# Kernel optimization log

Measured on AMD Instinct MI355X. Metric: run time of the kernel, lower is better.

Reference implementation:

```python
import jax, jax.numpy as jnp
import numpy as np

N = 65536
E = 524288
G = 8192
HID = 512


def setup_inputs() -> dict:
    key = jax.random.key(0)
    ks = jax.random.split(key, 10)
    v_x_raw = jax.random.normal(ks[0], (N, 3), dtype=jnp.float32)
    H_decoded = jax.random.normal(ks[1], (N, HID), dtype=jnp.float32)
    x_t = 2.0 * jax.random.normal(ks[2], (N, 3), dtype=jnp.float32)
    row = jax.random.randint(ks[3], (E,), 0, N)
    # avoid self edges (fully_connect_edges excludes i==j)
    col = (row + 1 + jax.random.randint(ks[4], (E,), 0, N - 1)) % N
    edges = jnp.stack([row, col]).astype(jnp.int64)
    gen_idx = (jnp.arange(G, dtype=jnp.int32) * (N // G)).astype(jnp.int32)
    gen_mask = jnp.zeros((N,), dtype=bool).at[gen_idx].set(True)
    W_proj = jax.random.normal(ks[5], (HID, HID // 2), dtype=jnp.float32) / np.sqrt(HID)
    b_proj = jnp.zeros((HID // 2,), dtype=jnp.float32)
    w_bond = jax.random.normal(ks[6], (HID // 2, 1), dtype=jnp.float32) / np.sqrt(HID // 2)
    b_bond = jnp.zeros((1,), dtype=jnp.float32)
    w_val = jax.random.normal(ks[7], (HID // 2, 1), dtype=jnp.float32) / np.sqrt(HID // 2)
    b_val = jnp.zeros((1,), dtype=jnp.float32)
    return {"v_x_raw": v_x_raw, "H_decoded": H_decoded, "x_t": x_t, "edges": edges,
            "gen_mask": gen_mask, "gen_idx": gen_idx, "W_proj": W_proj, "b_proj": b_proj,
            "w_bond": w_bond, "b_bond": b_bond, "w_val": w_val, "b_val": b_val}


def _constrained_velocity(v_x_raw, H_decoded, x_t, edges, gen_mask, gen_idx,
                          W_proj, b_proj, w_bond, b_bond, w_val, b_val):
    TARGET_LEN = 1.5   # target bond length
    MIN_DIST = 1.0     # clash cutoff
    EPS = 1e-8

    feat = H_decoded @ W_proj + b_proj                      # [N, HID//2]

    # --- bond length corrections: vectorized scatter-add over edges ---
    row, col = edges[0], edges[1]
    diff = x_t[row] - x_t[col]                              # [E, 3]
    dist = jnp.sqrt(jnp.maximum(jnp.sum(diff * diff, -1), 1e-24)) + EPS  # [E]
    edge_gate = (gen_mask[row] | gen_mask[col]).astype(x_t.dtype)
    # force_magnitude * force_direction = (d - L)/d * diff/d
    force = ((dist - TARGET_LEN) / (dist * dist) * edge_gate)[:, None] * diff  # [E,3]
    bond_corr = jnp.zeros_like(x_t).at[row].add(force).at[col].add(-force)

    # --- clash corrections: dense pairwise over generated atoms ---
    xg = x_t[gen_idx]                                       # [G, 3]
    sq = jnp.sum(xg * xg, -1)                               # [G]
    d2 = sq[:, None] + sq[None, :] - 2.0 * (xg @ xg.T)      # [G, G]
    d = jnp.sqrt(jnp.maximum(d2, 1e-24)) + EPS
    pair_mask = (d < MIN_DIST) & ~jnp.eye(xg.shape[0], dtype=bool)
    # (min - d)/d * (x_i - x_j)/d  ->  coef_ij * (x_i - x_j)
    coef = jnp.where(pair_mask, (MIN_DIST - d) / (d * d), 0.0)  # [G, G]
    corr_g = xg * jnp.sum(coef, 1, keepdims=True) - coef @ xg   # [G, 3]
    clash_corr = jnp.zeros_like(x_t).at[gen_idx].add(corr_g)

    bond_w = jax.nn.sigmoid(feat @ w_bond + b_bond)         # [N, 1]
    clash_w = jax.nn.sigmoid(feat @ w_val + b_val)          # [N, 1]
    return v_x_raw - 0.1 * bond_w * bond_corr - 0.05 * clash_w * clash_corr


def reference(v_x_raw, H_decoded, x_t, edges, gen_mask, gen_idx,
              W_proj, b_proj, w_bond, b_bond, w_val, b_val):
    return _constrained_velocity(v_x_raw, H_decoded, x_t, edges, gen_mask, gen_idx,
                                 W_proj, b_proj, w_bond, b_bond, w_val, b_val)
```

## Files before the change

kernel.cpp:

```cpp
#include <hip/hip_runtime.h>
#include <math.h>

#define HID_DIM  512
#define HIDH_DIM 256
#define ZBLOCKS  125
#define UBLOCKS  128
#define JC       256

__device__ __forceinline__ float dot4(float4 a, float4 b) {
    return a.x * b.x + a.y * b.y + a.z * b.z + a.w * b.w;
}

__global__ __launch_bounds__(256) void prep_kernel(
        const unsigned int* __restrict__ ew,
        const float* __restrict__ Wp,  const float* __restrict__ bp,
        const float* __restrict__ wb,  const float* __restrict__ bb,
        const float* __restrict__ wv,  const float* __restrict__ bv,
        const int* __restrict__ gen_idx, const float* __restrict__ x_t,
        float4* __restrict__ zbase, int zcount,
        float* __restrict__ u_bond, float* __restrict__ u_val,
        float* __restrict__ cvals, int* __restrict__ flag,
        float* __restrict__ xgx, float* __restrict__ xgy, float* __restrict__ xgz,
        unsigned char* __restrict__ mask, int* __restrict__ gpos,
        int n, int G, int GB) {
    int b = blockIdx.x, t = threadIdx.x;
    if (b < ZBLOCKS) {
        const float4 z = make_float4(0.f, 0.f, 0.f, 0.f);
        for (int i = b * 256 + t; i < zcount; i += ZBLOCKS * 256) zbase[i] = z;
    } else if (b == ZBLOCKS) {
        if (t < 64) {
            unsigned int v = ew[2 * t + 1];
            unsigned long long bl = __ballot(v == 0u);
            if (t == 0) flag[0] = (bl == 0xFFFFFFFFFFFFFFFFULL) ? 1 : 0;
        }
        __shared__ float s1[256], s2[256];
        float p1 = (t < HIDH_DIM) ? bp[t] * wb[t] : 0.f;
        float p2 = (t < HIDH_DIM) ? bp[t] * wv[t] : 0.f;
        s1[t] = p1; s2[t] = p2;
        __syncthreads();
        for (int s = 128; s > 0; s >>= 1) {
            if (t < s) { s1[t] += s1[t + s]; s2[t] += s2[t + s]; }
            __syncthreads();
        }
        if (t == 0) { cvals[0] = s1[0] + bb[0]; cvals[1] = s2[0] + bv[0]; }
    } else if (b < ZBLOCKS + 1 + UBLOCKS) {
        int w = t >> 6, lane = t & 63;
        int k = (b - ZBLOCKS - 1) * 4 + w;
        if (k < HID_DIM) {
            const float* wrow = Wp + (size_t)k * HIDH_DIM;
            float4 wr = *reinterpret_cast<const float4*>(wrow + lane * 4);
            float4 vb = *reinterpret_cast<const float4*>(wb + lane * 4);
            float4 vv = *reinterpret_cast<const float4*>(wv + lane * 4);
            float ub = dot4(wr, vb);
            float uv = dot4(wr, vv);
            #pragma unroll
            for (int off = 32; off > 0; off >>= 1) {
                ub += __shfl_down(ub, off, 64);
                uv += __shfl_down(uv, off, 64);
            }
            if (lane == 0) { u_bond[k] = ub; u_val[k] = uv; }
        }
    } else if (b < ZBLOCKS + 1 + UBLOCKS + GB) {
        int g = (b - ZBLOCKS - 1 - UBLOCKS) * 256 + t;
        if (g < G) {
            int idx = gen_idx[g];
            xgx[g] = x_t[3 * idx + 0];
            xgy[g] = x_t[3 * idx + 1];
            xgz[g] = x_t[3 * idx + 2];
        }
    } else {
        int base = ((b - ZBLOCKS - 1 - UBLOCKS - GB) * 256 + t) * 8;
        for (int k = 0; k < 8; ++k) {
            int i = base + k;
            if (i >= n) break;
            int lo = 0, hi = G - 1, g = -1;
            while (lo <= hi) {
                int mid = (lo + hi) >> 1;
                int v = gen_idx[mid];
                if (v == i) { g = mid; break; }
                if (v < i) lo = mid + 1; else hi = mid - 1;
            }
            mask[i] = (g >= 0) ? 1 : 0;
            if (g >= 0) gpos[i] = g;
        }
    }
}

__global__ __launch_bounds__(256) void mega_kernel(
        const float* __restrict__ H,
        const float* __restrict__ u_bond, const float* __restrict__ u_val,
        const float* __restrict__ cvals,
        const unsigned int* __restrict__ ew, const int* __restrict__ flag_p,
        const float* __restrict__ x_t, const unsigned char* __restrict__ mask,
        const float* __restrict__ xgx, const float* __restrict__ xgy,
        const float* __restrict__ xgz,
        float* __restrict__ bond_corr,
        float4* __restrict__ partials,
        float* __restrict__ bond_w, float* __restrict__ clash_w,
        int n, int E, int G, int NBG, int NBB, int NBC, int CXB) {
    __shared__ __align__(16) float sx[JC];
    __shared__ __align__(16) float sy[JC];
    __shared__ __align__(16) float sz[JC];
    int b = blockIdx.x, t = threadIdx.x;
    int stripe = b / 5, role = b - stripe * 5;

    if (role < 2) {
        int bb = stripe * 2 + role;
        if (bb >= NBG) return;
        int w = t >> 6, lane = t & 63;
        int row0 = bb * 32 + w * 8;
        int o0 = lane * 4, o1 = 256 + lane * 4;
        float4 ub0 = *reinterpret_cast<const float4*>(u_bond + o0);
        float4 ub1 = *reinterpret_cast<const float4*>(u_bond + o1);
        float4 uv0 = *reinterpret_cast<const float4*>(u_val + o0);
        float4 uv1 = *reinterpret_cast<const float4*>(u_val + o1);
        float c0 = cvals[0], c1 = cvals[1];
        #pragma unroll
        for (int r = 0; r < 8; r += 2) {
            int ra = row0 + r, rb = ra + 1;
            bool va = (ra < n), vb = (rb < n);
            const float* ha = H + (size_t)(va ? ra : 0) * HID_DIM;
            const float* hb = H + (size_t)(vb ? rb : 0) * HID_DIM;
            float4 a0 = *reinterpret_cast<const float4*>(ha + o0);
            float4 a1 = *reinterpret_cast<const float4*>(ha + o1);
            float4 b0 = *reinterpret_cast<const float4*>(hb + o0);
            float4 b1 = *reinterpret_cast<const float4*>(hb + o1);
            float sba = dot4(a0, ub0) + dot4(a1, ub1);
            float sva = dot4(a0, uv0) + dot4(a1, uv1);
            float sbb = dot4(b0, ub0) + dot4(b1, ub1);
            float svb = dot4(b0, uv0) + dot4(b1, uv1);
            #pragma unroll
            for (int off = 32; off > 0; off >>= 1) {
                sba += __shfl_down(sba, off, 64);
                sva += __shfl_down(sva, off, 64);
                sbb += __shfl_down(sbb, off, 64);
                svb += __shfl_down(svb, off, 64);
            }
            if (lane == 0) {
                if (va) {
                    bond_w[ra]  = 1.f / (1.f + expf(-(sba + c0)));
                    clash_w[ra] = 1.f / (1.f + expf(-(sva + c1)));
                }
                if (vb) {
                    bond_w[rb]  = 1.f / (1.f + expf(-(sbb + c0)));
                    clash_w[rb] = 1.f / (1.f + expf(-(svb + c1)));
                }
            }
        }
    } else if (role < 4) {
        int e = (stripe * 2 + role - 2) * 256 + t;
        if (e >= E) return;
        int f = flag_p[0];
        int row, col;
        if (f) {
            row = (int)ew[2 * (size_t)e];
            col = (int)ew[2 * ((size_t)E + e)];
        } else {
            row = (int)ew[e];
            col = (int)ew[(size_t)E + e];
        }
        if ((unsigned)row >= (unsigned)n || (unsigned)col >= (unsigned)n) return;
        if (!(mask[row] | mask[col])) return;
        float dx = x_t[3 * row + 0] - x_t[3 * col + 0];
        float dy = x_t[3 * row + 1] - x_t[3 * col + 1];
        float dz = x_t[3 * row + 2] - x_t[3 * col + 2];
        float d2 = dx * dx + dy * dy + dz * dz;
        float dist = sqrtf(fmaxf(d2, 1e-24f)) + 1e-8f;
        float s = (dist - 1.5f) / (dist * dist);
        float fx = s * dx, fy = s * dy, fz = s * dz;
        atomicAdd(&bond_corr[3 * row + 0],  fx);
        atomicAdd(&bond_corr[3 * row + 1],  fy);
        atomicAdd(&bond_corr[3 * row + 2],  fz);
        atomicAdd(&bond_corr[3 * col + 0], -fx);
        atomicAdd(&bond_corr[3 * col + 1], -fy);
        atomicAdd(&bond_corr[3 * col + 2], -fz);
    } else {
        int b2 = stripe;
        if (b2 >= NBC) return;
        int yc = b2 / CXB;
        int i  = (b2 - yc * CXB) * 256 + t;
        int j  = yc * JC + t;
        sx[t] = (j < G) ? xgx[j] : 1e30f;
        sy[t] = (j < G) ? xgy[j] : 1e30f;
        sz[t] = (j < G) ? xgz[j] : 1e30f;
        __syncthreads();
        if (i >= G) return;
        float xi = xgx[i], yi = xgy[i], zi = xgz[i];
        float csum = 0.f, cx = 0.f, cy = 0.f, cz = 0.f;
#define PROC(XS, YS, ZS) do {                                           \
            float dx = xi - (XS), dy = yi - (YS), dz = zi - (ZS);       \
            float d2 = fmaf(dx, dx, fmaf(dy, dy, dz * dz));             \
            float rm = __builtin_amdgcn_rsqf(d2);                       \
            float coef = fmaxf(fmaf(rm, rm, -rm), 0.0f);                \
            csum += coef;                                               \
            cx = fmaf(coef, (XS), cx);                                  \
            cy = fmaf(coef, (YS), cy);                                  \
            cz = fmaf(coef, (ZS), cz);                                  \
        } while (0)
        #pragma unroll 4
        for (int tt = 0; tt < JC; tt += 4) {
            float4 ax = *reinterpret_cast<const float4*>(&sx[tt]);
            float4 ay = *reinterpret_cast<const float4*>(&sy[tt]);
            float4 az = *reinterpret_cast<const float4*>(&sz[tt]);
            PROC(ax.x, ay.x, az.x);
            PROC(ax.y, ay.y, az.y);
            PROC(ax.z, ay.z, az.z);
            PROC(ax.w, ay.w, az.w);
        }
#undef PROC
        partials[(size_t)yc * G + i] = make_float4(csum, cx, cy, cz);
    }
}

__global__ void final_kernel(const float* __restrict__ v_x,
                             const float* __restrict__ bond_w,
                             const float* __restrict__ clash_w,
                             const float* __restrict__ bond_corr,
                             const unsigned char* __restrict__ mask,
                             const int* __restrict__ gpos,
                             const float* __restrict__ xgx,
                             const float* __restrict__ xgy,
                             const float* __restrict__ xgz,
                             const float4* __restrict__ partials,
                             float* __restrict__ out, int n, int G, int NYC) {
    int i = blockIdx.x * blockDim.x + threadIdx.x;
    if (i >= n) return;
    float bw = 0.1f * bond_w[i];
    float ox = v_x[3 * i + 0] - bw * bond_corr[3 * i + 0];
    float oy = v_x[3 * i + 1] - bw * bond_corr[3 * i + 1];
    float oz = v_x[3 * i + 2] - bw * bond_corr[3 * i + 2];
    if (mask[i]) {
        int g = gpos[i];
        float s = 0.f, vx = 0.f, vy = 0.f, vz = 0.f;
        for (int yc = 0; yc < NYC; ++yc) {
            float4 p = partials[(size_t)yc * G + g];
            s += p.x; vx += p.y; vy += p.z; vz += p.w;
        }
        float cw = 0.05f * clash_w[i];
        ox -= cw * (xgx[g] * s - vx);
        oy -= cw * (xgy[g] * s - vy);
        oz -= cw * (xgz[g] * s - vz);
    }
    out[3 * i + 0] = ox;
    out[3 * i + 1] = oy;
    out[3 * i + 2] = oz;
}

extern "C" void kernel_launch(void* const* d_in, const int* in_sizes, int n_in,
                              void* d_out, int out_size, void* d_ws, size_t ws_size,
                              hipStream_t stream) {
    const float* v_x_raw = (const float*)d_in[0];
    const float* H       = (const float*)d_in[1];
    const float* x_t     = (const float*)d_in[2];
    const unsigned int* edges_w = (const unsigned int*)d_in[3];
    const int* gen_idx   = (const int*)d_in[5];
    const float* W_proj  = (const float*)d_in[6];
    const float* b_proj  = (const float*)d_in[7];
    const float* w_bond  = (const float*)d_in[8];
    const float* b_bond  = (const float*)d_in[9];
    const float* w_val   = (const float*)d_in[10];
    const float* b_val   = (const float*)d_in[11];

    const int n = in_sizes[0] / 3;
    const int E = in_sizes[3] / 2;
    const int G = in_sizes[5];
    const int GB  = (G + 255) / 256;
    const int NYC = (G + JC - 1) / JC;

    char* ws = (char*)d_ws;
    float* bond_corr = (float*)(ws);
    size_t zbytes = (size_t)n * 12;
    size_t off = (zbytes + 15) & ~(size_t)15;
    int zcount = (int)(off / 16);
    unsigned char* mask = (unsigned char*)(ws + off); off += ((size_t)n + 15) & ~(size_t)15;
    int*   gpos    = (int*)(ws + off);                off += (size_t)n * 4;
    float* bond_w  = (float*)(ws + off);              off += (size_t)n * 4;
    float* clash_w = (float*)(ws + off);              off += (size_t)n * 4;
    float* u_bond  = (float*)(ws + off);              off += HID_DIM * 4;
    float* u_val   = (float*)(ws + off);              off += HID_DIM * 4;
    float* cvals   = (float*)(ws + off);              off += 16;
    int*   flag    = (int*)(ws + off);                off += 16;
    float* xgx     = (float*)(ws + off);              off += (size_t)G * 4;
    float* xgy     = (float*)(ws + off);              off += (size_t)G * 4;
    float* xgz     = (float*)(ws + off);              off += (size_t)G * 4;
    float4* partials = (float4*)(ws + off);           off += (size_t)NYC * G * 16;

    const int MB  = (n + 2047) / 2048;
    const int CXB = GB;
    const int NBC = CXB * NYC;
    const int NBG = (n + 31) / 32;
    const int NBB = (E + 255) / 256;

    int S = (NBG + 1) / 2;
    if ((NBB + 1) / 2 > S) S = (NBB + 1) / 2;
    if (NBC > S) S = NBC;

    prep_kernel<<<ZBLOCKS + 1 + UBLOCKS + GB + MB, 256, 0, stream>>>(
        edges_w, W_proj, b_proj, w_bond, b_bond, w_val, b_val,
        gen_idx, x_t, (float4*)ws, zcount,
        u_bond, u_val, cvals, flag, xgx, xgy, xgz, mask, gpos, n, G, GB);

    mega_kernel<<<S * 5, 256, 0, stream>>>(
        H, u_bond, u_val, cvals, edges_w, flag, x_t, mask,
        xgx, xgy, xgz, bond_corr, partials, bond_w, clash_w,
        n, E, G, NBG, NBB, NBC, CXB);

    final_kernel<<<(n + 255) / 256, 256, 0, stream>>>(
        v_x_raw, bond_w, clash_w, bond_corr, mask, gpos,
        xgx, xgy, xgz, partials, (float*)d_out, n, G, NYC);
}
```

Measured before the change: 98.86 us.

## Split gate GEMV out of mega kernel and rebalance bond/clash block interleave

Moves the H·u gate dot-products out of the interleaved mega kernel into a separate gate_kernel that uses half-wave (32-lane) reductions, with one row per half-wave and 8 rows per block. The remaining bond-scatter and clash work is interleaved 4:2 per stripe instead of 2:2:1. This separates the bandwidth-bound H stream from the atomic- and compute-heavy work so each gets its own launch shape. The cost is an extra kernel launch, and the gate pass is now serialized with the bond/clash pass instead of running concurrently with it.

Result: slower. 111.4 us (+12.7%).

```diff
diff --git a/kernel.cpp b/kernel.cpp
--- a/kernel.cpp
+++ b/kernel.cpp
@@ -86,69 +86,60 @@
     }
 }
 
-__global__ __launch_bounds__(256) void mega_kernel(
+__global__ __launch_bounds__(256) void gate_kernel(
         const float* __restrict__ H,
         const float* __restrict__ u_bond, const float* __restrict__ u_val,
         const float* __restrict__ cvals,
+        float* __restrict__ bond_w, float* __restrict__ clash_w, int n) {
+    int t = threadIdx.x, w = t >> 6, lane = t & 63;
+    int half = lane >> 5, l = lane & 31;
+    int row = blockIdx.x * 8 + w * 2 + half;
+    if (row >= n) return;
+    const float* h = H + (size_t)row * HID_DIM;
+    int o = l * 4;
+    float4 h0 = *reinterpret_cast<const float4*>(h + o);
+    float4 h1 = *reinterpret_cast<const float4*>(h + o + 128);
+    float4 h2 = *reinterpret_cast<const float4*>(h + o + 256);
+    float4 h3 = *reinterpret_cast<const float4*>(h + o + 384);
+    float4 ub0 = *reinterpret_cast<const float4*>(u_bond + o);
+    float4 ub1 = *reinterpret_cast<const float4*>(u_bond + o + 128);
+    float4 ub2 = *reinterpret_cast<const float4*>(u_bond + o + 256);
+    float4 ub3 = *reinterpret_cast<const float4*>(u_bond + o + 384);
+    float4 uv0 = *reinterpret_cast<const float4*>(u_val + o);
+    float4 uv1 = *reinterpret_cast<const float4*>(u_val + o + 128);
+    float4 uv2 = *reinterpret_cast<const float4*>(u_val + o + 256);
+    float4 uv3 = *reinterpret_cast<const float4*>(u_val + o + 384);
+    float sb = dot4(h0, ub0) + dot4(h1, ub1) + dot4(h2, ub2) + dot4(h3, ub3);
+    float sv = dot4(h0, uv0) + dot4(h1, uv1) + dot4(h2, uv2) + dot4(h3, uv3);
+    #pragma unroll
+    for (int off = 16; off > 0; off >>= 1) {
+        sb += __shfl_down(sb, off, 32);
+        sv += __shfl_down(sv, off, 32);
+    }
+    if (l == 0) {
+        bond_w[row]  = 1.f / (1.f + expf(-(sb + cvals[0])));
+        clash_w[row] = 1.f / (1.f + expf(-(sv + cvals[1])));
+    }
+}
+
+__global__ __launch_bounds__(256) void bondclash_kernel(
         const unsigned int* __restrict__ ew, const int* __restrict__ flag_p,
         const float* __restrict__ x_t, const unsigned char* __restrict__ mask,
         const float* __restrict__ xgx, const float* __restrict__ xgy,
         const float* __restrict__ xgz,
         float* __restrict__ bond_corr,
         float4* __restrict__ partials,
-        float* __restrict__ bond_w, float* __restrict__ clash_w,
-        int n, int E, int G, int NBG, int NBB, int NBC, int CXB) {
+        int n, int E, int G, int NBB, int NBC, int CXB) {
     __shared__ __align__(16) float sx[JC];
     __shared__ __align__(16) float sy[JC];
     __shared__ __align__(16) float sz[JC];
     int b = blockIdx.x, t = threadIdx.x;
-    int stripe = b / 5, role = b - stripe * 5;
-
-    if (role < 2) {
-        int bb = stripe * 2 + role;
-        if (bb >= NBG) return;
-        int w = t >> 6, lane = t & 63;
-        int row0 = bb * 32 + w * 8;
-        int o0 = lane * 4, o1 = 256 + lane * 4;
-        float4 ub0 = *reinterpret_cast<const float4*>(u_bond + o0);
-        float4 ub1 = *reinterpret_cast<const float4*>(u_bond + o1);
-        float4 uv0 = *reinterpret_cast<const float4*>(u_val + o0);
-        float4 uv1 = *reinterpret_cast<const float4*>(u_val + o1);
-        float c0 = cvals[0], c1 = cvals[1];
-        #pragma unroll
-        for (int r = 0; r < 8; r += 2) {
-            int ra = row0 + r, rb = ra + 1;
-            bool va = (ra < n), vb = (rb < n);
-            const float* ha = H + (size_t)(va ? ra : 0) * HID_DIM;
-            const float* hb = H + (size_t)(vb ? rb : 0) * HID_DIM;
-            float4 a0 = *reinterpret_cast<const float4*>(ha + o0);
-            float4 a1 = *reinterpret_cast<const float4*>(ha + o1);
-            float4 b0 = *reinterpret_cast<const float4*>(hb + o0);
-            float4 b1 = *reinterpret_cast<const float4*>(hb + o1);
-            float sba = dot4(a0, ub0) + dot4(a1, ub1);
-            float sva = dot4(a0, uv0) + dot4(a1, uv1);
-            float sbb = dot4(b0, ub0) + dot4(b1, ub1);
-            float svb = dot4(b0, uv0) + dot4(b1, uv1);
-            #pragma unroll
-            for (int off = 32; off > 0; off >>= 1) {
-                sba += __shfl_down(sba, off, 64);
-                sva += __shfl_down(sva, off, 64);
-                sbb += __shfl_down(sbb, off, 64);
-                svb += __shfl_down(svb, off, 64);
-            }
-            if (lane == 0) {
-                if (va) {
-                    bond_w[ra]  = 1.f / (1.f + expf(-(sba + c0)));
-                    clash_w[ra] = 1.f / (1.f + expf(-(sva + c1)));
-                }
-                if (vb) {
-                    bond_w[rb]  = 1.f / (1.f + expf(-(sbb + c0)));
-                    clash_w[rb] = 1.f / (1.f + expf(-(svb + c1)));
-                }
-            }
-        }
-    } else if (role < 4) {
-        int e = (stripe * 2 + role - 2) * 256 + t;
+    int stripe = b / 6, role = b - stripe * 6;
+
+    if (role < 4) {
+        int eb = stripe * 4 + role;
+        if (eb >= NBB) return;
+        int e = eb * 256 + t;
         if (e >= E) return;
         int f = flag_p[0];
         int row, col;
@@ -175,7 +166,7 @@
         atomicAdd(&bond_corr[3 * col + 1], -fy);
         atomicAdd(&bond_corr[3 * col + 2], -fz);
     } else {
-        int b2 = stripe;
+        int b2 = stripe * 2 + (role - 4);
         if (b2 >= NBC) return;
         int yc = b2 / CXB;
         int i  = (b2 - yc * CXB) * 256 + t;
@@ -288,22 +279,22 @@
     const int MB  = (n + 2047) / 2048;
     const int CXB = GB;
     const int NBC = CXB * NYC;
-    const int NBG = (n + 31) / 32;
     const int NBB = (E + 255) / 256;
 
-    int S = (NBG + 1) / 2;
-    if ((NBB + 1) / 2 > S) S = (NBB + 1) / 2;
-    if (NBC > S) S = NBC;
+    int S = (NBB + 3) / 4;
+    if ((NBC + 1) / 2 > S) S = (NBC + 1) / 2;
 
     prep_kernel<<<ZBLOCKS + 1 + UBLOCKS + GB + MB, 256, 0, stream>>>(
         edges_w, W_proj, b_proj, w_bond, b_bond, w_val, b_val,
         gen_idx, x_t, (float4*)ws, zcount,
         u_bond, u_val, cvals, flag, xgx, xgy, xgz, mask, gpos, n, G, GB);
 
-    mega_kernel<<<S * 5, 256, 0, stream>>>(
-        H, u_bond, u_val, cvals, edges_w, flag, x_t, mask,
-        xgx, xgy, xgz, bond_corr, partials, bond_w, clash_w,
-        n, E, G, NBG, NBB, NBC, CXB);
+    gate_kernel<<<(n + 7) / 8, 256, 0, stream>>>(
+        H, u_bond, u_val, cvals, bond_w, clash_w, n);
+
+    bondclash_kernel<<<S * 6, 256, 0, stream>>>(
+        edges_w, flag, x_t, mask, xgx, xgy, xgz,
+        bond_corr, partials, n, E, G, NBB, NBC, CXB);
 
     final_kernel<<<(n + 255) / 256, 256, 0, stream>>>(
         v_x_raw, bond_w, clash_w, bond_corr, mask, gpos,
```
